# Performance work log

Measured on AMD Instinct MI355X. Metric: run time of the kernel, lower is better.

## Reference

```python
import jax, jax.numpy as jnp
import numpy as np


def setup_inputs() -> dict:
    key = jax.random.key(0)
    B, T, FFT, HOP = 16, 2048, 1024, 256
    n_bins = FFT // 2 + 1  # 513
    stfts = jax.random.normal(key, (B, T, n_bins, 2), dtype=jnp.float32)
    return {"stfts": stfts, "frame_length": FFT, "frame_step": HOP, "fft_length": FFT}


def reference(stfts, frame_length, frame_step, fft_length):
    # --- precomputed constants (built in the layer's build()) ---
    n = jnp.arange(fft_length, dtype=jnp.float32)
    angles = (2.0 * np.pi / fft_length) * (n[:, None] * n[None, :])  # [fft, fft]
    idft_cos = jnp.cos(angles)
    idft_sin = jnp.sin(angles)
    # periodic Hann window
    t = jnp.arange(frame_length, dtype=jnp.float32)
    window = 0.5 - 0.5 * jnp.cos(2.0 * np.pi * t / frame_length)
    hop_ratio = frame_step / frame_length
    normalization = np.sqrt(1.0 / (1.0 - hop_ratio + 1e-8))
    syn_window = window / np.float32(normalization)
    if fft_length > frame_length:
        syn_window = jnp.pad(syn_window, (0, fft_length - frame_length))

    # --- forward ---
    real_part = stfts[..., 0]  # [B, T, n_bins]
    imag_part = stfts[..., 1]
    if fft_length % 2 == 0:
        mirror_real = real_part[:, :, 1:-1]
        mirror_imag = imag_part[:, :, 1:-1]
    else:
        mirror_real = real_part[:, :, 1:]
        mirror_imag = imag_part[:, :, 1:]
    full_real = jnp.concatenate([real_part, mirror_real[:, :, ::-1]], axis=-1)   # [B, T, fft]
    full_imag = jnp.concatenate([imag_part, -mirror_imag[:, :, ::-1]], axis=-1)  # [B, T, fft]

    # explicit IDFT via dense matmul (transpose_b in TF; matrices are symmetric)
    time_real = jnp.einsum('btf,nf->btn', full_real, idft_cos)
    time_real = time_real - jnp.einsum('btf,nf->btn', full_imag, idft_sin)
    time_real = time_real / jnp.float32(fft_length)

    windowed = (time_real * syn_window[None, None, :])[:, :, :frame_length]  # [B, T, frame_length]

    # overlap-and-add
    B, T, L = windowed.shape
    out_len = (T - 1) * frame_step + frame_length
    idx = jnp.arange(T)[:, None] * frame_step + jnp.arange(L)[None, :]  # [T, L]
    out = jnp.zeros((B, out_len), dtype=windowed.dtype).at[:, idx].add(windowed)
    return out
```

## Files before the change

### kernel.cpp

```cpp
#include <hip/hip_runtime.h>
#include <hip/hip_bf16.h>
#include <math.h>


#define BATCH  16
#define TFR    2048
#define FFTN   1024
#define HOP    256
#define OUTLEN 525056
#define M_TOT  (BATCH * TFR)
#define K_TOT  1026
#define K_PAD  1056
#define NKT    33
#define BM     128
#define BN     128
#define BK     32

#define STEP 6.13592315e-3f

typedef __attribute__((ext_vector_type(4))) float f32x4;
typedef __attribute__((ext_vector_type(8))) short bf16x8;

__global__ __launch_bounds__(256)
void build_B(__hip_bfloat16* __restrict__ Bg)
{
    const int n = blockIdx.x;
    const float window = 0.5f - 0.5f * cosf((float)n * STEP);
    const float scale  = window * 0.8660254f * (1.0f / (float)FFTN);

    for (int k = threadIdx.x; k < K_PAD; k += 256) {
        float val = 0.f;
        if (k < K_TOT) {
            const int f = k >> 1;
            const float ang = (float)((n * f) & (FFTN - 1)) * STEP;
            float s, c;
            sincosf(ang, &s, &c);
            if ((k & 1) == 0) {
                const float wr = (f == 0 || f == 512) ? 1.f : 2.f;
                val = wr * c * scale;
            } else {
                val = -2.f * s * scale;
            }
        }
        Bg[(size_t)n * K_PAD + k] = __float2bfloat16(val);
    }
}

__global__ __launch_bounds__(256)
void istft_gemm(const float* __restrict__ A, const __hip_bfloat16* __restrict__ Bg,
                float* __restrict__ out)
{
    __shared__ __hip_bfloat16 Asl[BM * BK];
    __shared__ __hip_bfloat16 Bsl[BN * BK];

    const int tid  = threadIdx.x;
    const int m0   = blockIdx.x * BM;
    const int n0   = blockIdx.y * BN;
    const int lane = tid & 63;
    const int wave = tid >> 6;
    const int wm   = wave >> 1;
    const int wn   = wave & 1;

    f32x4 acc[4][4] = {};

    const int sr = tid >> 4;
    const int sc = tid & 15;
    const int br = tid >> 1;
    const int bc = (tid & 1) * 16;

    const int fr = lane & 15;
    const int fk = (lane >> 4) * 8;

    for (int kt = 0; kt < NKT; ++kt) {
        #pragma unroll
        for (int r = 0; r < 8; ++r) {
            const int m    = r * 16 + sr;
            const int fidx = kt * 16 + sc;
            float2 v = make_float2(0.f, 0.f);
            if (fidx <= 512)
                v = *reinterpret_cast<const float2*>(A + (size_t)(m0 + m) * K_TOT + fidx * 2);
            __hip_bfloat162 h = __float22bfloat162_rn(v);
            *reinterpret_cast<__hip_bfloat162*>(&Asl[m * BK + sc * 2]) = h;
        }
        {
            const __hip_bfloat16* bg = Bg + (size_t)(n0 + br) * K_PAD + kt * BK + bc;
            *reinterpret_cast<bf16x8*>(&Bsl[br * BK + bc]) =
                *reinterpret_cast<const bf16x8*>(bg);
            *reinterpret_cast<bf16x8*>(&Bsl[br * BK + bc + 8]) =
                *reinterpret_cast<const bf16x8*>(bg + 8);
        }
        __syncthreads();

        bf16x8 a[4], b[4];
        #pragma unroll
        for (int mi = 0; mi < 4; ++mi)
            a[mi] = *reinterpret_cast<const bf16x8*>(&Asl[(wm * 64 + mi * 16 + fr) * BK + fk]);
        #pragma unroll
        for (int ni = 0; ni < 4; ++ni)
            b[ni] = *reinterpret_cast<const bf16x8*>(&Bsl[(wn * 64 + ni * 16 + fr) * BK + fk]);

        #pragma unroll
        for (int mi = 0; mi < 4; ++mi)
            #pragma unroll
            for (int ni = 0; ni < 4; ++ni)
                acc[mi][ni] = __builtin_amdgcn_mfma_f32_16x16x32_bf16(
                    a[mi], b[ni], acc[mi][ni], 0, 0, 0);

        __syncthreads();
    }

    const int cr = (lane >> 4) * 4;
    const int cc = lane & 15;
    #pragma unroll
    for (int mi = 0; mi < 4; ++mi) {
        #pragma unroll
        for (int ni = 0; ni < 4; ++ni) {
            const int n = n0 + wn * 64 + ni * 16 + cc;
            #pragma unroll
            for (int j = 0; j < 4; ++j) {
                const int m = m0 + wm * 64 + mi * 16 + cr + j;
                const int bb = m >> 11;
                const int t  = m & (TFR - 1);
                atomicAdd(out + (size_t)bb * OUTLEN + t * HOP + n, acc[mi][ni][j]);
            }
        }
    }
}

extern "C" void kernel_launch(void* const* d_in, const int* in_sizes, int n_in,
                              void* d_out, int out_size, void* d_ws, size_t ws_size,
                              hipStream_t stream)
{
    const float* A = reinterpret_cast<const float*>(d_in[0]);
    float* out = reinterpret_cast<float*>(d_out);
    __hip_bfloat16* Bg = reinterpret_cast<__hip_bfloat16*>(d_ws);

    hipMemsetAsync(d_out, 0, (size_t)out_size * sizeof(float), stream);

    build_B<<<dim3(FFTN), dim3(256), 0, stream>>>(Bg);

    dim3 grid(M_TOT / BM, FFTN / BN);
    istft_gemm<<<grid, dim3(256), 0, stream>>>(A, Bg, out);
}
```

Before: 242.8 us.

## Pre-convert A to padded bf16 and stream tiles via global_load_lds

Adds a separate pass that converts the fp32 interleaved spectrogram into a padded bf16 matrix in workspace. The GEMM then loads A and B tiles straight into LDS with 16-byte global_load_lds, instead of doing per-element fp32 loads and conversion inside the main loop. The aim is to cut the VGPR and VALU cost of staging inside the GEMM. In exchange it adds an extra kernel and a round trip of about 69MB through memory, and it falls back to the old kernel when the workspace is too small.

```diff
diff --git a/kernel.cpp b/kernel.cpp
--- a/kernel.cpp
+++ b/kernel.cpp
@@ -15,11 +15,19 @@
 #define BM     128
 #define BN     128
 #define BK     32
+#define CHUNKS_PER_ROW (K_PAD / 8)
 
 #define STEP 6.13592315e-3f
 
 typedef __attribute__((ext_vector_type(4))) float f32x4;
 typedef __attribute__((ext_vector_type(8))) short bf16x8;
+
+__device__ __forceinline__ void load_lds16(const void* g, void* l)
+{
+    __builtin_amdgcn_global_load_lds((const __attribute__((address_space(1))) void*)g,
+                                     (__attribute__((address_space(3))) void*)l,
+                                     16, 0, 0);
+}
 
 __global__ __launch_bounds__(256)
 void build_B(__hip_bfloat16* __restrict__ Bg)
@@ -47,8 +55,29 @@
 }
 
 __global__ __launch_bounds__(256)
-void istft_gemm(const float* __restrict__ A, const __hip_bfloat16* __restrict__ Bg,
-                float* __restrict__ out)
+void convert_A(const float* __restrict__ A, __hip_bfloat16* __restrict__ Ab)
+{
+    const int idx = blockIdx.x * 256 + threadIdx.x;
+    if (idx >= M_TOT * CHUNKS_PER_ROW) return;
+    const int m  = idx / CHUNKS_PER_ROW;
+    const int k8 = (idx - m * CHUNKS_PER_ROW) * 8;
+
+    const float* src = A + (size_t)m * K_TOT + k8;
+    union { bf16x8 v; __hip_bfloat162 h[4]; } u;
+    #pragma unroll
+    for (int j = 0; j < 8; j += 2) {
+        float2 t = make_float2(0.f, 0.f);
+        if (k8 + j < K_TOT)
+            t = *reinterpret_cast<const float2*>(src + j);
+        u.h[j >> 1] = __float22bfloat162_rn(t);
+    }
+    *reinterpret_cast<bf16x8*>(Ab + (size_t)m * K_PAD + k8) = u.v;
+}
+
+__global__ __launch_bounds__(256)
+void istft_gemm_lds(const __hip_bfloat16* __restrict__ Ab,
+                    const __hip_bfloat16* __restrict__ Bg,
+                    float* __restrict__ out)
 {
     __shared__ __hip_bfloat16 Asl[BM * BK];
     __shared__ __hip_bfloat16 Bsl[BN * BK];
@@ -63,11 +92,82 @@
 
     f32x4 acc[4][4] = {};
 
+    const int sm = tid >> 2;
+    const int sk = (tid & 3) * 8;
+
+    const int fr = lane & 15;
+    const int fk = (lane >> 4) * 8;
+
+    const __hip_bfloat16* ga0 = Ab + (size_t)(m0 + sm) * K_PAD + sk;
+    const __hip_bfloat16* ga1 = Ab + (size_t)(m0 + 64 + sm) * K_PAD + sk;
+    const __hip_bfloat16* gb0 = Bg + (size_t)(n0 + sm) * K_PAD + sk;
+    const __hip_bfloat16* gb1 = Bg + (size_t)(n0 + 64 + sm) * K_PAD + sk;
+
+    for (int kt = 0; kt < NKT; ++kt) {
+        const int ko = kt * BK;
+        load_lds16(ga0 + ko, Asl + tid * 8);
+        load_lds16(ga1 + ko, Asl + 2048 + tid * 8);
+        load_lds16(gb0 + ko, Bsl + tid * 8);
+        load_lds16(gb1 + ko, Bsl + 2048 + tid * 8);
+        __syncthreads();
+
+        bf16x8 a[4], b[4];
+        #pragma unroll
+        for (int mi = 0; mi < 4; ++mi)
+            a[mi] = *reinterpret_cast<const bf16x8*>(&Asl[(wm * 64 + mi * 16 + fr) * BK + fk]);
+        #pragma unroll
+        for (int ni = 0; ni < 4; ++ni)
+            b[ni] = *reinterpret_cast<const bf16x8*>(&Bsl[(wn * 64 + ni * 16 + fr) * BK + fk]);
+
+        #pragma unroll
+        for (int mi = 0; mi < 4; ++mi)
+            #pragma unroll
+            for (int ni = 0; ni < 4; ++ni)
+                acc[mi][ni] = __builtin_amdgcn_mfma_f32_16x16x32_bf16(
+                    a[mi], b[ni], acc[mi][ni], 0, 0, 0);
+
+        __syncthreads();
+    }
+
+    const int cr = (lane >> 4) * 4;
+    const int cc = lane & 15;
+    #pragma unroll
+    for (int mi = 0; mi < 4; ++mi) {
+        #pragma unroll
+        for (int ni = 0; ni < 4; ++ni) {
+            const int n = n0 + wn * 64 + ni * 16 + cc;
+            #pragma unroll
+            for (int j = 0; j < 4; ++j) {
+                const int m = m0 + wm * 64 + mi * 16 + cr + j;
+                const int bb = m >> 11;
+                const int t  = m & (TFR - 1);
+                atomicAdd(out + (size_t)bb * OUTLEN + t * HOP + n, acc[mi][ni][j]);
+            }
+        }
+    }
+}
+
+__global__ __launch_bounds__(256)
+void istft_gemm_fb(const float* __restrict__ A, const __hip_bfloat16* __restrict__ Bg,
+                   float* __restrict__ out)
+{
+    __shared__ __hip_bfloat16 Asl[BM * BK];
+    __shared__ __hip_bfloat16 Bsl[BN * BK];
+
+    const int tid  = threadIdx.x;
+    const int m0   = blockIdx.x * BM;
+    const int n0   = blockIdx.y * BN;
+    const int lane = tid & 63;
+    const int wave = tid >> 6;
+    const int wm   = wave >> 1;
+    const int wn   = wave & 1;
+
+    f32x4 acc[4][4] = {};
+
     const int sr = tid >> 4;
     const int sc = tid & 15;
     const int br = tid >> 1;
     const int bc = (tid & 1) * 16;
-
     const int fr = lane & 15;
     const int fk = (lane >> 4) * 8;
 
@@ -133,12 +233,24 @@
 {
     const float* A = reinterpret_cast<const float*>(d_in[0]);
     float* out = reinterpret_cast<float*>(d_out);
-    __hip_bfloat16* Bg = reinterpret_cast<__hip_bfloat16*>(d_ws);
+
+    const size_t abBytes = (size_t)M_TOT * K_PAD * sizeof(__hip_bfloat16);
+    const size_t bBytes  = (size_t)FFTN * K_PAD * sizeof(__hip_bfloat16);
 
     hipMemsetAsync(d_out, 0, (size_t)out_size * sizeof(float), stream);
 
-    build_B<<<dim3(FFTN), dim3(256), 0, stream>>>(Bg);
-
     dim3 grid(M_TOT / BM, FFTN / BN);
-    istft_gemm<<<grid, dim3(256), 0, stream>>>(A, Bg, out);
-}
+
+    if (ws_size >= abBytes + bBytes) {
+        __hip_bfloat16* Ab = reinterpret_cast<__hip_bfloat16*>(d_ws);
+        __hip_bfloat16* Bg = reinterpret_cast<__hip_bfloat16*>((char*)d_ws + abBytes);
+        build_B<<<dim3(FFTN), dim3(256), 0, stream>>>(Bg);
+        const int nChunks = M_TOT * CHUNKS_PER_ROW;
+        convert_A<<<dim3((nChunks + 255) / 256), dim3(256), 0, stream>>>(A, Ab);
+        istft_gemm_lds<<<grid, dim3(256), 0, stream>>>(Ab, Bg, out);
+    } else {
+        __hip_bfloat16* Bg = reinterpret_cast<__hip_bfloat16*>(d_ws);
+        build_B<<<dim3(FFTN), dim3(256), 0, stream>>>(Bg);
+        istft_gemm_fb<<<grid, dim3(256), 0, stream>>>(A, Bg, out);
+    }
+}
```

Result: faster. 230.7 us (-5.0%).

## Fold overlap-add into GEMM K dimension and drop atomics

Applied to the files above, without the earlier changes.

Recasts the iSTFT so each output block of 256 samples is a single GEMM row. Its K dimension concatenates four consecutive padded bf16 frames, which works because the padded A rows are laid out contiguously, and the synthesis matrix B is built per shift. Each output element is written exactly once, so the zero-fill memset and the per-element float atomics go away. A separate pass converts the input to padded bf16, and the GEMM stages tiles straight into LDS with global_load_lds. The cost is an extra conversion pass over the input and a longer K loop, and the grid drops to fewer, longer blocks, which may leave CUs underused.

```diff
diff --git a/kernel.cpp b/kernel.cpp
--- a/kernel.cpp
+++ b/kernel.cpp
@@ -5,57 +5,108 @@
 
 #define BATCH  16
 #define TFR    2048
-#define FFTN   1024
+#define NB     513
 #define HOP    256
 #define OUTLEN 525056
-#define M_TOT  (BATCH * TFR)
-#define K_TOT  1026
-#define K_PAD  1056
-#define NKT    33
-#define BM     128
-#define BN     128
+#define RROWS  2051
+#define PBR    2054
+#define FSTR   1040
+#define KTOT   (4 * FSTR)
 #define BK     32
-
-#define STEP 6.13592315e-3f
+#define NKT    (KTOT / BK)
+#define KVAL   1026
+#define MT     17
+#define TOTROW (BATCH * PBR + 128)
+#define CHPR   (FSTR / 8)
 
 typedef __attribute__((ext_vector_type(4))) float f32x4;
 typedef __attribute__((ext_vector_type(8))) short bf16x8;
 
+__device__ __forceinline__ void load_lds16(const void* g, void* l)
+{
+    __builtin_amdgcn_global_load_lds((const __attribute__((address_space(1))) void*)g,
+                                     (__attribute__((address_space(3))) void*)l,
+                                     16, 0, 0);
+}
+
+#define STEP 6.13592315e-3f
+
 __global__ __launch_bounds__(256)
 void build_B(__hip_bfloat16* __restrict__ Bg)
 {
-    const int n = blockIdx.x;
-    const float window = 0.5f - 0.5f * cosf((float)n * STEP);
-    const float scale  = window * 0.8660254f * (1.0f / (float)FFTN);
+    __shared__ float cosT[1024];
+    __shared__ float sinT[1024];
+    const int j = blockIdx.x;
+    for (int i = threadIdx.x; i < 1024; i += 256) {
+        float s, c;
+        sincosf((float)i * STEP, &s, &c);
+        cosT[i] = c; sinT[i] = s;
+    }
+    __syncthreads();
 
-    for (int k = threadIdx.x; k < K_PAD; k += 256) {
+    for (int k = threadIdx.x; k < KTOT; k += 256) {
+        const int d  = k / FSTR;
+        const int kk = k - d * FSTR;
         float val = 0.f;
-        if (k < K_TOT) {
-            const int f = k >> 1;
-            const float ang = (float)((n * f) & (FFTN - 1)) * STEP;
-            float s, c;
-            sincosf(ang, &s, &c);
-            if ((k & 1) == 0) {
+        if (kk < KVAL) {
+            const int   f   = kk >> 1;
+            const int   n   = 768 - 256 * d + j;
+            const float syn = (0.5f - 0.5f * cosT[n]) * 0.8660254f * (1.0f / 1024.0f);
+            const int   idx = (n * f) & 1023;
+            if ((kk & 1) == 0) {
                 const float wr = (f == 0 || f == 512) ? 1.f : 2.f;
-                val = wr * c * scale;
+                val = wr * cosT[idx] * syn;
             } else {
-                val = -2.f * s * scale;
+                val = -2.f * sinT[idx] * syn;
             }
         }
-        Bg[(size_t)n * K_PAD + k] = __float2bfloat16(val);
+        Bg[(size_t)j * KTOT + k] = __float2bfloat16(val);
     }
 }
 
 __global__ __launch_bounds__(256)
-void istft_gemm(const float* __restrict__ A, const __hip_bfloat16* __restrict__ Bg,
-                float* __restrict__ out)
+void convert_A(const float* __restrict__ A, __hip_bfloat16* __restrict__ Ab)
 {
-    __shared__ __hip_bfloat16 Asl[BM * BK];
-    __shared__ __hip_bfloat16 Bsl[BN * BK];
+    const int idx = blockIdx.x * 256 + threadIdx.x;
+    if (idx >= TOTROW * CHPR) return;
+    const int row = idx / CHPR;
+    const int c8  = (idx - row * CHPR) * 8;
+
+    const int b  = row / PBR;
+    const int rr = row - b * PBR;
+    const bool valid = (b < BATCH) && (rr >= 3) && (rr < 3 + TFR);
+
+    union { bf16x8 v; __hip_bfloat162 h[4]; } u;
+    if (valid) {
+        const int t = rr - 3;
+        const float* src = A + (size_t)(b * TFR + t) * KVAL + c8;
+        #pragma unroll
+        for (int j = 0; j < 8; j += 2) {
+            float2 p = make_float2(0.f, 0.f);
+            if (c8 + j < KVAL)
+                p = *reinterpret_cast<const float2*>(src + j);
+            u.h[j >> 1] = __float22bfloat162_rn(p);
+        }
+    } else {
+        #pragma unroll
+        for (int j = 0; j < 4; ++j) u.h[j] = __float22bfloat162_rn(make_float2(0.f, 0.f));
+    }
+    *reinterpret_cast<bf16x8*>(Ab + (size_t)row * FSTR + c8) = u.v;
+}
+
+__global__ __launch_bounds__(256)
+void istft_gemm2(const __hip_bfloat16* __restrict__ Ab,
+                 const __hip_bfloat16* __restrict__ Bg,
+                 float* __restrict__ out)
+{
+    __shared__ __hip_bfloat16 Asl[128 * BK];
+    __shared__ __hip_bfloat16 Bsl[128 * BK];
 
     const int tid  = threadIdx.x;
-    const int m0   = blockIdx.x * BM;
-    const int n0   = blockIdx.y * BN;
+    const int bi   = blockIdx.x;
+    const int b    = bi / MT;
+    const int rt   = (bi - b * MT) * 128;
+    const int n0   = blockIdx.y * 128;
     const int lane = tid & 63;
     const int wave = tid >> 6;
     const int wm   = wave >> 1;
@@ -63,48 +114,38 @@
 
     f32x4 acc[4][4] = {};
 
-    const int sr = tid >> 4;
-    const int sc = tid & 15;
-    const int br = tid >> 1;
-    const int bc = (tid & 1) * 16;
-
+    const int sm = tid >> 2;
+    const int sk = (tid & 3) * 8;
     const int fr = lane & 15;
     const int fk = (lane >> 4) * 8;
 
+    const __hip_bfloat16* ga0 = Ab + ((size_t)b * PBR + rt + sm) * FSTR + sk;
+    const __hip_bfloat16* ga1 = Ab + ((size_t)b * PBR + rt + 64 + sm) * FSTR + sk;
+    const __hip_bfloat16* gb0 = Bg + (size_t)(n0 + sm) * KTOT + sk;
+    const __hip_bfloat16* gb1 = Bg + (size_t)(n0 + 64 + sm) * KTOT + sk;
+
     for (int kt = 0; kt < NKT; ++kt) {
-        #pragma unroll
-        for (int r = 0; r < 8; ++r) {
-            const int m    = r * 16 + sr;
-            const int fidx = kt * 16 + sc;
-            float2 v = make_float2(0.f, 0.f);
-            if (fidx <= 512)
-                v = *reinterpret_cast<const float2*>(A + (size_t)(m0 + m) * K_TOT + fidx * 2);
-            __hip_bfloat162 h = __float22bfloat162_rn(v);
-            *reinterpret_cast<__hip_bfloat162*>(&Asl[m * BK + sc * 2]) = h;
-        }
-        {
-            const __hip_bfloat16* bg = Bg + (size_t)(n0 + br) * K_PAD + kt * BK + bc;
-            *reinterpret_cast<bf16x8*>(&Bsl[br * BK + bc]) =
-                *reinterpret_cast<const bf16x8*>(bg);
-            *reinterpret_cast<bf16x8*>(&Bsl[br * BK + bc + 8]) =
-                *reinterpret_cast<const bf16x8*>(bg + 8);
-        }
+        const int ko = kt * BK;
+        load_lds16(ga0 + ko, Asl + tid * 8);
+        load_lds16(ga1 + ko, Asl + 2048 + tid * 8);
+        load_lds16(gb0 + ko, Bsl + tid * 8);
+        load_lds16(gb1 + ko, Bsl + 2048 + tid * 8);
         __syncthreads();
 
-        bf16x8 a[4], b[4];
+        bf16x8 a[4], bv[4];
         #pragma unroll
         for (int mi = 0; mi < 4; ++mi)
             a[mi] = *reinterpret_cast<const bf16x8*>(&Asl[(wm * 64 + mi * 16 + fr) * BK + fk]);
         #pragma unroll
         for (int ni = 0; ni < 4; ++ni)
-            b[ni] = *reinterpret_cast<const bf16x8*>(&Bsl[(wn * 64 + ni * 16 + fr) * BK + fk]);
+            bv[ni] = *reinterpret_cast<const bf16x8*>(&Bsl[(wn * 64 + ni * 16 + fr) * BK + fk]);
 
         #pragma unroll
         for (int mi = 0; mi < 4; ++mi)
             #pragma unroll
             for (int ni = 0; ni < 4; ++ni)
                 acc[mi][ni] = __builtin_amdgcn_mfma_f32_16x16x32_bf16(
-                    a[mi], b[ni], acc[mi][ni], 0, 0, 0);
+                    a[mi], bv[ni], acc[mi][ni], 0, 0, 0);
 
         __syncthreads();
     }
@@ -115,13 +156,12 @@
     for (int mi = 0; mi < 4; ++mi) {
         #pragma unroll
         for (int ni = 0; ni < 4; ++ni) {
-            const int n = n0 + wn * 64 + ni * 16 + cc;
+            const int col = n0 + wn * 64 + ni * 16 + cc;
             #pragma unroll
             for (int j = 0; j < 4; ++j) {
-                const int m = m0 + wm * 64 + mi * 16 + cr + j;
-                const int bb = m >> 11;
-                const int t  = m & (TFR - 1);
-                atomicAdd(out + (size_t)bb * OUTLEN + t * HOP + n, acc[mi][ni][j]);
+                const int r = rt + wm * 64 + mi * 16 + cr + j;
+                if (r < RROWS)
+                    out[(size_t)b * OUTLEN + (size_t)r * 256 + col] = acc[mi][ni][j];
             }
         }
     }
@@ -133,12 +173,15 @@
 {
     const float* A = reinterpret_cast<const float*>(d_in[0]);
     float* out = reinterpret_cast<float*>(d_out);
-    __hip_bfloat16* Bg = reinterpret_cast<__hip_bfloat16*>(d_ws);
 
-    hipMemsetAsync(d_out, 0, (size_t)out_size * sizeof(float), stream);
+    const size_t abBytes = (size_t)TOTROW * FSTR * sizeof(__hip_bfloat16);
+    __hip_bfloat16* Ab = reinterpret_cast<__hip_bfloat16*>(d_ws);
+    __hip_bfloat16* Bg = reinterpret_cast<__hip_bfloat16*>((char*)d_ws + abBytes);
 
-    build_B<<<dim3(FFTN), dim3(256), 0, stream>>>(Bg);
+    build_B<<<dim3(256), dim3(256), 0, stream>>>(Bg);
 
-    dim3 grid(M_TOT / BM, FFTN / BN);
-    istft_gemm<<<grid, dim3(256), 0, stream>>>(A, Bg, out);
+    const int nChunks = TOTROW * CHPR;
+    convert_A<<<dim3((nChunks + 255) / 256), dim3(256), 0, stream>>>(A, Ab);
+
+    istft_gemm2<<<dim3(BATCH * MT, 2), dim3(256), 0, stream>>>(Ab, Bg, out);
 }
```

Result: faster. 235.6 us (-3.0%).
